# Kernel optimization log

Measured on AMD Instinct MI355X. Metric: run time of the kernel, lower is better.

The kernel has to match this reference:

```python
import math
import jax, jax.numpy as jnp
import numpy as np

N_HEAD = 16
LORA_SCALE = 16.0 / 8.0  # lora_alpha / r


def lora_linear(x, W, b, A, B):
    # y = x @ W^T + b + scale * (x @ A^T) @ B^T
    base = jnp.einsum('btc,oc->bto', x, W) + b
    low = jnp.einsum('btc,rc->btr', x, A)
    return base + LORA_SCALE * jnp.einsum('btr,or->bto', low, B)


def setup_inputs() -> dict:
    key = jax.random.key(0)
    ks = jax.random.split(key, 8)
    B, T, C = 2, 2048, 1024
    r = 8
    s = 0.02
    return {
        'x': jax.random.normal(ks[0], (B, T, C), jnp.float32),
        'W_attn': jax.random.normal(ks[1], (3 * C, C), jnp.float32) * s,
        'b_attn': jnp.zeros((3 * C,), jnp.float32),
        'A_attn': jax.random.normal(ks[2], (r, C), jnp.float32) * s,
        'B_attn': jax.random.normal(ks[3], (3 * C, r), jnp.float32) * s,
        'W_proj': jax.random.normal(ks[4], (C, C), jnp.float32) * s,
        'b_proj': jnp.zeros((C,), jnp.float32),
        'A_proj': jax.random.normal(ks[5], (r, C), jnp.float32) * s,
        'B_proj': jax.random.normal(ks[6], (C, r), jnp.float32) * s,
    }


def reference(x, W_attn, b_attn, A_attn, B_attn, W_proj, b_proj, A_proj, B_proj):
    B, T, C = x.shape
    H = N_HEAD
    hd = C // H
    qkv = lora_linear(x, W_attn, b_attn, A_attn, B_attn)  # [B,T,3C]
    q, k, v = jnp.split(qkv, 3, axis=2)
    # [B,H,T,hd]
    q = q.reshape(B, T, H, hd).transpose(0, 2, 1, 3)
    k = k.reshape(B, T, H, hd).transpose(0, 2, 1, 3)
    v = v.reshape(B, T, H, hd).transpose(0, 2, 1, 3)
    att = jnp.einsum('bhqd,bhkd->bhqk', q, k) * (1.0 / math.sqrt(hd))
    causal = jnp.tril(jnp.ones((T, T), bool))
    att = jnp.where(causal, att, -jnp.inf)
    att = jax.nn.softmax(att, axis=-1)
    out = jnp.einsum('bhqk,bhkd->bhqd', att, v)
    out = out.transpose(0, 2, 1, 3).reshape(B, T, C)
    return lora_linear(out, W_proj, b_proj, A_proj, B_proj)
```

## Files before the change

kernel.cpp:

```cpp
#include <hip/hip_runtime.h>
#include <hip/hip_bf16.h>
#include <stdint.h>

typedef __bf16 bf16_t;
typedef __bf16 bf16x8 __attribute__((ext_vector_type(8)));
typedef __bf16 bf16x4 __attribute__((ext_vector_type(4)));
typedef __bf16 bf16x2 __attribute__((ext_vector_type(2)));
typedef float f32x4 __attribute__((ext_vector_type(4)));
typedef float f32x16 __attribute__((ext_vector_type(16)));
typedef uint32_t u32;
typedef uint32_t u32x4 __attribute__((ext_vector_type(4)));

typedef __attribute__((address_space(1))) void as1void;
typedef __attribute__((address_space(3))) void as3void;

#define QSCALE 0.18033688011112042f

__constant__ unsigned char kOrder[24] = {7, 20, 22, 23, 6, 16, 18, 19, 21,
                                         5, 12, 14, 15, 17, 4, 8, 10, 11, 13,
                                         3, 9, 2, 1, 0};

__device__ __forceinline__ void gll16(const void* g, void* l) {
  __builtin_amdgcn_global_load_lds((as1void*)g, (as3void*)l, 16, 0, 0);
}

__device__ __forceinline__ u32 pack2(float a, float b) {
  bf16x2 t = {(bf16_t)a, (bf16_t)b};
  return __builtin_bit_cast(u32, t);
}

__global__ void prep_all(const float* __restrict__ W_attn, const float* __restrict__ B_attn,
                         const float* __restrict__ A_attn, const float* __restrict__ W_proj,
                         const float* __restrict__ B_proj, const float* __restrict__ A_proj,
                         const float4* __restrict__ x,
                         bf16_t* __restrict__ WaE, bf16_t* __restrict__ WpE,
                         bf16x4* __restrict__ Xb) {
  int bid = blockIdx.x;
  if (bid < 16384) {
    int idx = bid * 256 + threadIdx.x;
    const float *W, *Bm, *Am;
    bf16_t* dst;
    if (idx < 3145728) {
      W = W_attn; Bm = B_attn; Am = A_attn; dst = WaE;
    } else {
      idx -= 3145728;
      W = W_proj; Bm = B_proj; Am = A_proj; dst = WpE;
    }
    int o = idx >> 10, c = idx & 1023;
    float acc = W[idx];
#pragma unroll
    for (int r = 0; r < 8; ++r)
      acc += 2.0f * Bm[o * 8 + r] * Am[r * 1024 + c];
    dst[idx] = (bf16_t)acc;
  } else {
    int i = (bid - 16384) * 256 + threadIdx.x;
    float4 v = x[i];
    bf16x4 o = {(bf16_t)v.x, (bf16_t)v.y, (bf16_t)v.z, (bf16_t)v.w};
    Xb[i] = o;
  }
}

template <bool QKV>
__global__ __launch_bounds__(256, 3) void gemm_bt(
    const bf16_t* __restrict__ A, const bf16_t* __restrict__ Bt,
    const float* __restrict__ bias,
    bf16_t* __restrict__ Qb, bf16_t* __restrict__ Kb, bf16_t* __restrict__ Vb,
    float* __restrict__ Out) {
  __shared__ bf16_t Als[128][64];
  __shared__ bf16_t Bls[128][64];
  const int m0 = blockIdx.x * 128;
  const int n0 = blockIdx.y * 128;
  const int tid = threadIdx.x;
  const int lane = tid & 63;
  const int w = tid >> 6;
  const int wm = w >> 1, wn = w & 1;
  const int lr = lane & 15, g = lane >> 4;
  const int sw = (lane & 7) << 3;
  const int srow = lane >> 3;
  const int soff = ((lane & 7) ^ srow) * 8;

  f32x4 acc[4][4] = {};

  for (int k0 = 0; k0 < 1024; k0 += 64) {
#pragma unroll
    for (int c = 0; c < 4; ++c) {
      int r = w * 32 + c * 8 + srow;
      gll16(A + (size_t)(m0 + r) * 1024 + k0 + soff, &Als[w * 32 + c * 8][0]);
      gll16(Bt + (size_t)(n0 + r) * 1024 + k0 + soff, &Bls[w * 32 + c * 8][0]);
    }
    __syncthreads();
#pragma unroll
    for (int ks = 0; ks < 2; ++ks) {
      bf16x8 af[4], bfv[4];
#pragma unroll
      for (int i = 0; i < 4; ++i)
        af[i] = *(const bf16x8*)&Als[wm * 64 + i * 16 + lr][(ks * 32 + g * 8) ^ sw];
#pragma unroll
      for (int j = 0; j < 4; ++j)
        bfv[j] = *(const bf16x8*)&Bls[wn * 64 + j * 16 + lr][(ks * 32 + g * 8) ^ sw];
#pragma unroll
      for (int i = 0; i < 4; ++i)
#pragma unroll
        for (int j = 0; j < 4; ++j)
          acc[i][j] = __builtin_amdgcn_mfma_f32_16x16x32_bf16(af[i], bfv[j], acc[i][j], 0, 0, 0);
    }
    __syncthreads();
  }

#pragma unroll
  for (int i = 0; i < 4; ++i) {
#pragma unroll
    for (int j = 0; j < 4; ++j) {
#pragma unroll
      for (int e = 0; e < 4; ++e) {
        int m = m0 + wm * 64 + i * 16 + g * 4 + e;
        int n = n0 + wn * 64 + j * 16 + lr;
        float v = acc[i][j][e] + bias[n];
        if (QKV) {
          int b = m >> 11, t = m & 2047;
          int which = n >> 10, hn = n & 1023;
          int h = hn >> 6, d = hn & 63;
          if (which == 0) v *= QSCALE;
          bf16_t* dst = (which == 0) ? Qb : (which == 1) ? Kb : Vb;
          dst[(((size_t)(b * 16 + h)) * 2048 + t) * 64 + d] = (bf16_t)v;
        } else {
          Out[(size_t)m * 1024 + n] = v;
        }
      }
    }
  }
}

__global__ __launch_bounds__(256, 2) void attn_fwd(
    const bf16_t* __restrict__ Qb, const bf16_t* __restrict__ Kb,
    const bf16_t* __restrict__ Vb, bf16_t* __restrict__ Ob,
    bf16_t* __restrict__ Po, float* __restrict__ Pml) {
  __shared__ bf16_t Kls[2][128][64];
  __shared__ bf16_t Vt[2][64][128];

  int id = blockIdx.x;
  int xcd = id & 7, r = id >> 3;
  int bh = xcd * 4 + (r & 3);
  int j = kOrder[r >> 2];
  int qb, kt0, kt1, part;
  if (j < 8) {
    qb = j; kt0 = 0; kt1 = qb + 1; part = -1;
  } else {
    qb = 8 + ((j - 8) >> 1);
    part = (j - 8) & 1;
    int kts = qb + 1, nA = (kts + 1) >> 1;
    kt0 = part ? nA : 0;
    kt1 = part ? kts : nA;
  }
  int b = bh >> 4, h = bh & 15;

  const int tid = threadIdx.x, lane = tid & 63, w = tid >> 6;
  const int q32 = lane & 31;
  const int hi = lane >> 5;
  const int ksw = (q32 & 7) << 3;
  const int vkey = ((q32 & 7) ^ (q32 >> 2)) << 3;
  const bf16_t* Qp = Qb + (size_t)bh * 2048 * 64;
  const bf16_t* Kp = Kb + (size_t)bh * 2048 * 64;
  const bf16_t* Vp = Vb + (size_t)bh * 2048 * 64;

  const int q0 = qb * 128;
  const int qrow = q0 + w * 32 + q32;

  const int kbase = (tid >> 4) * 8;
  const int dbase = (tid & 15) * 4;
  const int ksr = lane >> 3;
  const int kso = ((lane & 7) ^ ksr) * 8;

  bf16x8 qf[4];
#pragma unroll
  for (int ds = 0; ds < 4; ++ds)
    qf[ds] = *(const bf16x8*)(Qp + (size_t)qrow * 64 + ds * 16 + hi * 8);

  float m_run = -3e38f, l_run = 0.f;
  f32x16 o_acc[2] = {};

  {
    const int kp = kt0 * 128;
    uint2 rowv[8];
#pragma unroll
    for (int rr = 0; rr < 8; ++rr)
      rowv[rr] = *(const uint2*)(Vp + (size_t)(kp + kbase + rr) * 64 + dbase);
#pragma unroll
    for (int c = 0; c < 4; ++c) {
      int rb = w * 32 + c * 8;
      gll16(Kp + (size_t)(kp + rb + ksr) * 64 + kso, &Kls[0][rb][0]);
    }
#pragma unroll
    for (int dd = 0; dd < 4; ++dd) {
      u32 sel = (dd & 1) ? 0x07060302u : 0x05040100u;
      u32 a0 = (dd >> 1) ? rowv[0].y : rowv[0].x;
      u32 a1 = (dd >> 1) ? rowv[1].y : rowv[1].x;
      u32 a2 = (dd >> 1) ? rowv[2].y : rowv[2].x;
      u32 a3 = (dd >> 1) ? rowv[3].y : rowv[3].x;
      u32 a4 = (dd >> 1) ? rowv[4].y : rowv[4].x;
      u32 a5 = (dd >> 1) ? rowv[5].y : rowv[5].x;
      u32 a6 = (dd >> 1) ? rowv[6].y : rowv[6].x;
      u32 a7 = (dd >> 1) ? rowv[7].y : rowv[7].x;
      int4 val;
      val.x = __builtin_amdgcn_perm(a1, a0, sel);
      val.y = __builtin_amdgcn_perm(a3, a2, sel);
      val.z = __builtin_amdgcn_perm(a5, a4, sel);
      val.w = __builtin_amdgcn_perm(a7, a6, sel);
      int d = dbase + dd;
      int key = ((d & 7) ^ ((d >> 2) & 7)) << 3;
      *(int4*)&Vt[0][d][kbase ^ key] = val;
    }
    __syncthreads();
  }

  int cb = 0;
  for (int kt = kt0; kt < kt1; ++kt) {
    const bool haveNext = (kt + 1 < kt1);
    const bool maskt = (kt == qb);
    const int nfa = maskt ? (w + 1) : 4;
    const int nb = cb ^ 1;

    uint2 rowv[8];
    if (haveNext) {
      const int kn = (kt + 1) * 128;
#pragma unroll
      for (int rr = 0; rr < 8; ++rr)
        rowv[rr] = *(const uint2*)(Vp + (size_t)(kn + kbase + rr) * 64 + dbase);
#pragma unroll
      for (int c = 0; c < 4; ++c) {
        int rb = w * 32 + c * 8;
        gll16(Kp + (size_t)(kn + rb + ksr) * 64 + kso, &Kls[nb][rb][0]);
      }
    }

    f32x16 s[4] = {};
    __builtin_amdgcn_s_setprio(1);
#pragma unroll
    for (int fa = 0; fa < 4; ++fa) {
      if (fa < nfa) {
#pragma unroll
        for (int ds = 0; ds < 4; ++ds) {
          bf16x8 kf = *(const bf16x8*)&Kls[cb][fa * 32 + q32][(ds * 16 + hi * 8) ^ ksw];
          s[fa] = __builtin_amdgcn_mfma_f32_32x32x16_bf16(kf, qf[ds], s[fa], 0, 0, 0);
        }
      }
    }
    __builtin_amdgcn_s_setprio(0);

    float mloc = -3e38f;
#pragma unroll
    for (int fa = 0; fa < 4; ++fa) {
      if (fa < nfa) {
        if (maskt && fa == w) {
#pragma unroll
          for (int rr = 0; rr < 16; ++rr) {
            int km = (rr & 3) + 8 * (rr >> 2) + 4 * hi;
            if (km > q32) s[fa][rr] = -3e38f;
          }
        }
#pragma unroll
        for (int rr = 0; rr < 16; ++rr) mloc = fmaxf(mloc, s[fa][rr]);
      }
    }
    mloc = fmaxf(mloc, __shfl_xor(mloc, 32, 64));
    if (!__all(mloc <= m_run + 8.0f)) {
      float mnew = fmaxf(m_run, mloc);
      float rs = __builtin_amdgcn_exp2f(m_run - mnew);
      m_run = mnew;
      l_run *= rs;
      o_acc[0] *= rs;
      o_acc[1] *= rs;
    }

    if (haveNext) {
#pragma unroll
      for (int dd = 0; dd < 4; ++dd) {
        u32 sel = (dd & 1) ? 0x07060302u : 0x05040100u;
        u32 a0 = (dd >> 1) ? rowv[0].y : rowv[0].x;
        u32 a1 = (dd >> 1) ? rowv[1].y : rowv[1].x;
        u32 a2 = (dd >> 1) ? rowv[2].y : rowv[2].x;
        u32 a3 = (dd >> 1) ? rowv[3].y : rowv[3].x;
        u32 a4 = (dd >> 1) ? rowv[4].y : rowv[4].x;
        u32 a5 = (dd >> 1) ? rowv[5].y : rowv[5].x;
        u32 a6 = (dd >> 1) ? rowv[6].y : rowv[6].x;
        u32 a7 = (dd >> 1) ? rowv[7].y : rowv[7].x;
        int4 val;
        val.x = __builtin_amdgcn_perm(a1, a0, sel);
        val.y = __builtin_amdgcn_perm(a3, a2, sel);
        val.z = __builtin_amdgcn_perm(a5, a4, sel);
        val.w = __builtin_amdgcn_perm(a7, a6, sel);
        int d = dbase + dd;
        int key = ((d & 7) ^ ((d >> 2) & 7)) << 3;
        *(int4*)&Vt[nb][d][kbase ^ key] = val;
      }
    }

    float lsum = 0.f;
#pragma unroll
    for (int fa = 0; fa < 4; ++fa) {
      if (fa < nfa) {
        float p[16];
#pragma unroll
        for (int rr = 0; rr < 16; ++rr) {
          p[rr] = __builtin_amdgcn_exp2f(s[fa][rr] - m_run);
          lsum += p[rr];
        }
        u32 x0 = pack2(p[0], p[1]),   x1 = pack2(p[2], p[3]);
        u32 x2 = pack2(p[4], p[5]),   x3 = pack2(p[6], p[7]);
        u32 y0 = pack2(p[8], p[9]),   y1 = pack2(p[10], p[11]);
        u32 y2 = pack2(p[12], p[13]), y3 = pack2(p[14], p[15]);
        u32 z0 = hi ? x0 : x2;
        u32 z1 = hi ? x1 : x3;
        u32 z2 = hi ? y0 : y2;
        u32 z3 = hi ? y1 : y3;
        z0 = (u32)__shfl_xor((int)z0, 32, 64);
        z1 = (u32)__shfl_xor((int)z1, 32, 64);
        z2 = (u32)__shfl_xor((int)z2, 32, 64);
        z3 = (u32)__shfl_xor((int)z3, 32, 64);
        u32x4 pw0 = hi ? (u32x4){z0, z1, x2, x3} : (u32x4){x0, x1, z0, z1};
        u32x4 pw1 = hi ? (u32x4){z2, z3, y2, y3} : (u32x4){y0, y1, z2, z3};
        bf16x8 P0 = __builtin_bit_cast(bf16x8, pw0);
        bf16x8 P1 = __builtin_bit_cast(bf16x8, pw1);
        __builtin_amdgcn_s_setprio(1);
#pragma unroll
        for (int db = 0; db < 2; ++db) {
          int d = db * 32 + q32;
          bf16x8 vf0 = *(const bf16x8*)&Vt[cb][d][(fa * 32 + hi * 8) ^ vkey];
          o_acc[db] = __builtin_amdgcn_mfma_f32_32x32x16_bf16(vf0, P0, o_acc[db], 0, 0, 0);
          bf16x8 vf1 = *(const bf16x8*)&Vt[cb][d][(fa * 32 + 16 + hi * 8) ^ vkey];
          o_acc[db] = __builtin_amdgcn_mfma_f32_32x32x16_bf16(vf1, P1, o_acc[db], 0, 0, 0);
        }
        __builtin_amdgcn_s_setprio(0);
      }
    }
    lsum += __shfl_xor(lsum, 32, 64);
    l_run += lsum;

    __syncthreads();
    cb = nb;
  }

  if (part < 0) {
    float inv = 1.0f / l_run;
    bf16_t* obase = Ob + ((size_t)(b * 2048 + qrow)) * 1024 + h * 64;
#pragma unroll
    for (int db = 0; db < 2; ++db) {
#pragma unroll
      for (int rg = 0; rg < 4; ++rg) {
        bf16x4 ov = {(bf16_t)(o_acc[db][rg * 4 + 0] * inv),
                     (bf16_t)(o_acc[db][rg * 4 + 1] * inv),
                     (bf16_t)(o_acc[db][rg * 4 + 2] * inv),
                     (bf16_t)(o_acc[db][rg * 4 + 3] * inv)};
        *(bf16x4*)(obase + db * 32 + rg * 8 + hi * 4) = ov;
      }
    }
  } else {
    int sidx = bh * 16 + (qb - 8) * 2 + part;
    int prow = w * 32 + q32;
    bf16_t* po = Po + (size_t)sidx * 8192 + prow * 64;
#pragma unroll
    for (int db = 0; db < 2; ++db) {
#pragma unroll
      for (int rg = 0; rg < 4; ++rg) {
        bf16x4 ov = {(bf16_t)o_acc[db][rg * 4 + 0], (bf16_t)o_acc[db][rg * 4 + 1],
                     (bf16_t)o_acc[db][rg * 4 + 2], (bf16_t)o_acc[db][rg * 4 + 3]};
        *(bf16x4*)(po + db * 32 + rg * 8 + hi * 4) = ov;
      }
    }
    if (hi == 0) {
      Pml[sidx * 256 + prow * 2] = m_run;
      Pml[sidx * 256 + prow * 2 + 1] = l_run;
    }
  }
}

__global__ __launch_bounds__(256) void attn_merge(
    const bf16_t* __restrict__ Po, const float* __restrict__ Pml,
    bf16_t* __restrict__ Ob) {
  int blk = blockIdx.x;
  int bh = blk >> 3, qb8 = blk & 7;
  int qb = 8 + qb8;
  int b = bh >> 4, h = bh & 15;
  int sA = bh * 16 + qb8 * 2, sB = sA + 1;
  int t = threadIdx.x;
  int row = t >> 1, c0 = (t & 1) * 32;

  float mA = Pml[sA * 256 + row * 2], lA = Pml[sA * 256 + row * 2 + 1];
  float mB = Pml[sB * 256 + row * 2], lB = Pml[sB * 256 + row * 2 + 1];
  float m = fmaxf(mA, mB);
  float wA = __builtin_amdgcn_exp2f(mA - m);
  float wB = __builtin_amdgcn_exp2f(mB - m);
  float inv = 1.0f / (lA * wA + lB * wB);
  wA *= inv;
  wB *= inv;

  const bf16_t* pa = Po + (size_t)sA * 8192 + row * 64 + c0;
  const bf16_t* pb = Po + (size_t)sB * 8192 + row * 64 + c0;
  bf16_t* ob = Ob + ((size_t)(b * 2048 + qb * 128 + row)) * 1024 + h * 64 + c0;
#pragma unroll
  for (int u = 0; u < 4; ++u) {
    bf16x8 a = *(const bf16x8*)(pa + u * 8);
    bf16x8 c = *(const bf16x8*)(pb + u * 8);
    bf16x8 o;
#pragma unroll
    for (int i = 0; i < 8; ++i)
      o[i] = (bf16_t)((float)a[i] * wA + (float)c[i] * wB);
    *(bf16x8*)(ob + u * 8) = o;
  }
}

extern "C" void kernel_launch(void* const* d_in, const int* in_sizes, int n_in,
                              void* d_out, int out_size, void* d_ws, size_t ws_size,
                              hipStream_t stream) {
  const float* x      = (const float*)d_in[0];
  const float* W_attn = (const float*)d_in[1];
  const float* b_attn = (const float*)d_in[2];
  const float* A_attn = (const float*)d_in[3];
  const float* B_attn = (const float*)d_in[4];
  const float* W_proj = (const float*)d_in[5];
  const float* b_proj = (const float*)d_in[6];
  const float* A_proj = (const float*)d_in[7];
  const float* B_proj = (const float*)d_in[8];
  float* out = (float*)d_out;

  char* ws = (char*)d_ws;
  bf16_t* WaE = (bf16_t*)(ws);
  bf16_t* WpE = (bf16_t*)(ws + 6291456);
  bf16_t* Xb  = (bf16_t*)(ws + 8388608);
  bf16_t* Qb  = (bf16_t*)(ws + 16777216);
  bf16_t* Kb  = (bf16_t*)(ws + 25165824);
  bf16_t* Vb  = (bf16_t*)(ws + 33554432);
  bf16_t* Ob  = (bf16_t*)(ws + 41943040);
  float*  Pml = (float*)(ws);
  bf16_t* Po  = (bf16_t*)(ws + 8388608);

  prep_all<<<20480, 256, 0, stream>>>(W_attn, B_attn, A_attn, W_proj, B_proj, A_proj,
                                      (const float4*)x, WaE, WpE, (bf16x4*)Xb);

  gemm_bt<true><<<dim3(32, 24), 256, 0, stream>>>(Xb, WaE, b_attn, Qb, Kb, Vb, nullptr);
  attn_fwd<<<768, 256, 0, stream>>>(Qb, Kb, Vb, Ob, Po, Pml);
  attn_merge<<<256, 256, 0, stream>>>(Po, Pml, Ob);
  gemm_bt<false><<<dim3(32, 8), 256, 0, stream>>>(Ob, WpE, b_proj, nullptr, nullptr, nullptr, out);
}
```

Measured before the change: 113.0 us.

## Enlarge attention query tile to 256 rows with 512-thread blocks

Attention blocks now process 256 query rows using 8 waves instead of 128 rows with 4 waves. Each staged K/V tile is reused by twice as many queries, so global and LDS traffic per query drops. Causal masking, split-KV partitioning, the V transpose layout and the merge kernel are all adapted to the new tile size. The trade-offs are fewer blocks, more work on diagonal tiles where waves sit idle, and higher register and occupancy pressure.

```diff
diff --git a/kernel.cpp b/kernel.cpp
--- a/kernel.cpp
+++ b/kernel.cpp
@@ -16,9 +16,7 @@
 
 #define QSCALE 0.18033688011112042f
 
-__constant__ unsigned char kOrder[24] = {7, 20, 22, 23, 6, 16, 18, 19, 21,
-                                         5, 12, 14, 15, 17, 4, 8, 10, 11, 13,
-                                         3, 9, 2, 1, 0};
+__constant__ unsigned char kOrder12[12] = {3, 10, 11, 8, 9, 2, 6, 7, 4, 5, 1, 0};
 
 __device__ __forceinline__ void gll16(const void* g, void* l) {
   __builtin_amdgcn_global_load_lds((as1void*)g, (as3void*)l, 16, 0, 0);
@@ -131,7 +129,7 @@
   }
 }
 
-__global__ __launch_bounds__(256, 2) void attn_fwd(
+__global__ __launch_bounds__(512, 4) void attn_fwd(
     const bf16_t* __restrict__ Qb, const bf16_t* __restrict__ Kb,
     const bf16_t* __restrict__ Vb, bf16_t* __restrict__ Ob,
     bf16_t* __restrict__ Po, float* __restrict__ Pml) {
@@ -141,16 +139,15 @@
   int id = blockIdx.x;
   int xcd = id & 7, r = id >> 3;
   int bh = xcd * 4 + (r & 3);
-  int j = kOrder[r >> 2];
+  int j = kOrder12[r >> 2];
   int qb, kt0, kt1, part;
-  if (j < 8) {
-    qb = j; kt0 = 0; kt1 = qb + 1; part = -1;
+  if (j < 4) {
+    qb = j; kt0 = 0; kt1 = 2 * qb + 2; part = -1;
   } else {
-    qb = 8 + ((j - 8) >> 1);
-    part = (j - 8) & 1;
-    int kts = qb + 1, nA = (kts + 1) >> 1;
-    kt0 = part ? nA : 0;
-    kt1 = part ? kts : nA;
+    qb = 4 + ((j - 4) >> 1);
+    part = (j - 4) & 1;
+    kt0 = part ? (qb + 1) : 0;
+    kt1 = part ? (2 * qb + 2) : (qb + 1);
   }
   int b = bh >> 4, h = bh & 15;
 
@@ -158,16 +155,16 @@
   const int q32 = lane & 31;
   const int hi = lane >> 5;
   const int ksw = (q32 & 7) << 3;
-  const int vkey = ((q32 & 7) ^ (q32 >> 2)) << 3;
+  const int vkey = ((q32 ^ (q32 >> 1)) & 7) << 3;
   const bf16_t* Qp = Qb + (size_t)bh * 2048 * 64;
   const bf16_t* Kp = Kb + (size_t)bh * 2048 * 64;
   const bf16_t* Vp = Vb + (size_t)bh * 2048 * 64;
 
-  const int q0 = qb * 128;
+  const int q0 = qb * 256;
   const int qrow = q0 + w * 32 + q32;
 
-  const int kbase = (tid >> 4) * 8;
-  const int dbase = (tid & 15) * 4;
+  const int kbase = (tid >> 5) * 8;
+  const int dbase = (tid & 31) * 2;
   const int ksr = lane >> 3;
   const int kso = ((lane & 7) ^ ksr) * 8;
 
@@ -181,33 +178,25 @@
 
   {
     const int kp = kt0 * 128;
-    uint2 rowv[8];
+    u32 rowv[8];
 #pragma unroll
     for (int rr = 0; rr < 8; ++rr)
-      rowv[rr] = *(const uint2*)(Vp + (size_t)(kp + kbase + rr) * 64 + dbase);
-#pragma unroll
-    for (int c = 0; c < 4; ++c) {
-      int rb = w * 32 + c * 8;
+      rowv[rr] = *(const u32*)(Vp + (size_t)(kp + kbase + rr) * 64 + dbase);
+#pragma unroll
+    for (int c = 0; c < 2; ++c) {
+      int rb = w * 16 + c * 8;
       gll16(Kp + (size_t)(kp + rb + ksr) * 64 + kso, &Kls[0][rb][0]);
     }
 #pragma unroll
-    for (int dd = 0; dd < 4; ++dd) {
-      u32 sel = (dd & 1) ? 0x07060302u : 0x05040100u;
-      u32 a0 = (dd >> 1) ? rowv[0].y : rowv[0].x;
-      u32 a1 = (dd >> 1) ? rowv[1].y : rowv[1].x;
-      u32 a2 = (dd >> 1) ? rowv[2].y : rowv[2].x;
-      u32 a3 = (dd >> 1) ? rowv[3].y : rowv[3].x;
-      u32 a4 = (dd >> 1) ? rowv[4].y : rowv[4].x;
-      u32 a5 = (dd >> 1) ? rowv[5].y : rowv[5].x;
-      u32 a6 = (dd >> 1) ? rowv[6].y : rowv[6].x;
-      u32 a7 = (dd >> 1) ? rowv[7].y : rowv[7].x;
+    for (int dd = 0; dd < 2; ++dd) {
+      u32 sel = dd ? 0x07060302u : 0x05040100u;
       int4 val;
-      val.x = __builtin_amdgcn_perm(a1, a0, sel);
-      val.y = __builtin_amdgcn_perm(a3, a2, sel);
-      val.z = __builtin_amdgcn_perm(a5, a4, sel);
-      val.w = __builtin_amdgcn_perm(a7, a6, sel);
+      val.x = __builtin_amdgcn_perm(rowv[1], rowv[0], sel);
+      val.y = __builtin_amdgcn_perm(rowv[3], rowv[2], sel);
+      val.z = __builtin_amdgcn_perm(rowv[5], rowv[4], sel);
+      val.w = __builtin_amdgcn_perm(rowv[7], rowv[6], sel);
       int d = dbase + dd;
-      int key = ((d & 7) ^ ((d >> 2) & 7)) << 3;
+      int key = ((d ^ (d >> 1)) & 7) << 3;
       *(int4*)&Vt[0][d][kbase ^ key] = val;
     }
     __syncthreads();
@@ -216,19 +205,24 @@
   int cb = 0;
   for (int kt = kt0; kt < kt1; ++kt) {
     const bool haveNext = (kt + 1 < kt1);
-    const bool maskt = (kt == qb);
-    const int nfa = maskt ? (w + 1) : 4;
+    const int dtile = kt - 2 * qb;
+    int nfa;
+    if (dtile < 0) nfa = 4;
+    else if (dtile == 0) nfa = (w < 4) ? (w + 1) : 4;
+    else nfa = (w < 4) ? 0 : (w - 3);
+    const int dfa = (dtile == 0) ? ((w < 4) ? w : -1)
+                                 : ((dtile == 1 && w >= 4) ? (w - 4) : -1);
     const int nb = cb ^ 1;
 
-    uint2 rowv[8];
+    u32 rowv[8];
     if (haveNext) {
       const int kn = (kt + 1) * 128;
 #pragma unroll
       for (int rr = 0; rr < 8; ++rr)
-        rowv[rr] = *(const uint2*)(Vp + (size_t)(kn + kbase + rr) * 64 + dbase);
-#pragma unroll
-      for (int c = 0; c < 4; ++c) {
-        int rb = w * 32 + c * 8;
+        rowv[rr] = *(const u32*)(Vp + (size_t)(kn + kbase + rr) * 64 + dbase);
+#pragma unroll
+      for (int c = 0; c < 2; ++c) {
+        int rb = w * 16 + c * 8;
         gll16(Kp + (size_t)(kn + rb + ksr) * 64 + kso, &Kls[nb][rb][0]);
       }
     }
@@ -251,7 +245,7 @@
 #pragma unroll
     for (int fa = 0; fa < 4; ++fa) {
       if (fa < nfa) {
-        if (maskt && fa == w) {
+        if (fa == dfa) {
 #pragma unroll
           for (int rr = 0; rr < 16; ++rr) {
             int km = (rr & 3) + 8 * (rr >> 2) + 4 * hi;
@@ -274,23 +268,15 @@
 
     if (haveNext) {
 #pragma unroll
-      for (int dd = 0; dd < 4; ++dd) {
-        u32 sel = (dd & 1) ? 0x07060302u : 0x05040100u;
-        u32 a0 = (dd >> 1) ? rowv[0].y : rowv[0].x;
-        u32 a1 = (dd >> 1) ? rowv[1].y : rowv[1].x;
-        u32 a2 = (dd >> 1) ? rowv[2].y : rowv[2].x;
-        u32 a3 = (dd >> 1) ? rowv[3].y : rowv[3].x;
-        u32 a4 = (dd >> 1) ? rowv[4].y : rowv[4].x;
-        u32 a5 = (dd >> 1) ? rowv[5].y : rowv[5].x;
-        u32 a6 = (dd >> 1) ? rowv[6].y : rowv[6].x;
-        u32 a7 = (dd >> 1) ? rowv[7].y : rowv[7].x;
+      for (int dd = 0; dd < 2; ++dd) {
+        u32 sel = dd ? 0x07060302u : 0x05040100u;
         int4 val;
-        val.x = __builtin_amdgcn_perm(a1, a0, sel);
-        val.y = __builtin_amdgcn_perm(a3, a2, sel);
-        val.z = __builtin_amdgcn_perm(a5, a4, sel);
-        val.w = __builtin_amdgcn_perm(a7, a6, sel);
+        val.x = __builtin_amdgcn_perm(rowv[1], rowv[0], sel);
+        val.y = __builtin_amdgcn_perm(rowv[3], rowv[2], sel);
+        val.z = __builtin_amdgcn_perm(rowv[5], rowv[4], sel);
+        val.w = __builtin_amdgcn_perm(rowv[7], rowv[6], sel);
         int d = dbase + dd;
-        int key = ((d & 7) ^ ((d >> 2) & 7)) << 3;
+        int key = ((d ^ (d >> 1)) & 7) << 3;
         *(int4*)&Vt[nb][d][kbase ^ key] = val;
       }
     }
@@ -355,9 +341,9 @@
       }
     }
   } else {
-    int sidx = bh * 16 + (qb - 8) * 2 + part;
+    int sidx = bh * 8 + (qb - 4) * 2 + part;
     int prow = w * 32 + q32;
-    bf16_t* po = Po + (size_t)sidx * 8192 + prow * 64;
+    bf16_t* po = Po + (size_t)sidx * 16384 + prow * 64;
 #pragma unroll
     for (int db = 0; db < 2; ++db) {
 #pragma unroll
@@ -368,8 +354,8 @@
       }
     }
     if (hi == 0) {
-      Pml[sidx * 256 + prow * 2] = m_run;
-      Pml[sidx * 256 + prow * 2 + 1] = l_run;
+      Pml[sidx * 512 + prow * 2] = m_run;
+      Pml[sidx * 512 + prow * 2 + 1] = l_run;
     }
   }
 }
@@ -378,15 +364,14 @@
     const bf16_t* __restrict__ Po, const float* __restrict__ Pml,
     bf16_t* __restrict__ Ob) {
   int blk = blockIdx.x;
-  int bh = blk >> 3, qb8 = blk & 7;
-  int qb = 8 + qb8;
+  int bh = blk >> 2, qb4 = blk & 3;
+  int qb = 4 + qb4;
   int b = bh >> 4, h = bh & 15;
-  int sA = bh * 16 + qb8 * 2, sB = sA + 1;
-  int t = threadIdx.x;
-  int row = t >> 1, c0 = (t & 1) * 32;
-
-  float mA = Pml[sA * 256 + row * 2], lA = Pml[sA * 256 + row * 2 + 1];
-  float mB = Pml[sB * 256 + row * 2], lB = Pml[sB * 256 + row * 2 + 1];
+  int sA = bh * 8 + qb4 * 2, sB = sA + 1;
+  int row = threadIdx.x;
+
+  float mA = Pml[sA * 512 + row * 2], lA = Pml[sA * 512 + row * 2 + 1];
+  float mB = Pml[sB * 512 + row * 2], lB = Pml[sB * 512 + row * 2 + 1];
   float m = fmaxf(mA, mB);
   float wA = __builtin_amdgcn_exp2f(mA - m);
   float wB = __builtin_amdgcn_exp2f(mB - m);
@@ -394,11 +379,11 @@
   wA *= inv;
   wB *= inv;
 
-  const bf16_t* pa = Po + (size_t)sA * 8192 + row * 64 + c0;
-  const bf16_t* pb = Po + (size_t)sB * 8192 + row * 64 + c0;
-  bf16_t* ob = Ob + ((size_t)(b * 2048 + qb * 128 + row)) * 1024 + h * 64 + c0;
-#pragma unroll
-  for (int u = 0; u < 4; ++u) {
+  const bf16_t* pa = Po + (size_t)sA * 16384 + row * 64;
+  const bf16_t* pb = Po + (size_t)sB * 16384 + row * 64;
+  bf16_t* ob = Ob + ((size_t)(b * 2048 + qb * 256 + row)) * 1024 + h * 64;
+#pragma unroll
+  for (int u = 0; u < 8; ++u) {
     bf16x8 a = *(const bf16x8*)(pa + u * 8);
     bf16x8 c = *(const bf16x8*)(pb + u * 8);
     bf16x8 o;
@@ -438,7 +423,7 @@
                                       (const float4*)x, WaE, WpE, (bf16x4*)Xb);
 
   gemm_bt<true><<<dim3(32, 24), 256, 0, stream>>>(Xb, WaE, b_attn, Qb, Kb, Vb, nullptr);
-  attn_fwd<<<768, 256, 0, stream>>>(Qb, Kb, Vb, Ob, Po, Pml);
-  attn_merge<<<256, 256, 0, stream>>>(Po, Pml, Ob);
+  attn_fwd<<<384, 512, 0, stream>>>(Qb, Kb, Vb, Ob, Po, Pml);
+  attn_merge<<<128, 256, 0, stream>>>(Po, Pml, Ob);
   gemm_bt<false><<<dim3(32, 8), 256, 0, stream>>>(Ob, WpE, b_proj, nullptr, nullptr, nullptr, out);
 }
```

After: 181.5 us. 60.6% more time.

## Pre-transpose V globally, DMA it into LDS, and XCD-aware GEMM tile mapping

Applied to the files above, without the earlier changes.

Adds a separate kernel that transposes V into a [bh][d][t] layout. The attention kernel can then load V tiles straight into LDS with global_load_lds instead of register loads plus perm shuffles. The GEMM grids become 1D with a block-to-tile mapping that groups tiles per XCD for L2 locality. The first split-attention partial is written directly into Ob, so the merge reads it back from there, which shrinks the Po scratch. The cost is an extra kernel launch and an extra pass over V through global memory.

```diff
diff --git a/kernel.cpp b/kernel.cpp
--- a/kernel.cpp
+++ b/kernel.cpp
@@ -60,6 +60,32 @@
   }
 }
 
+__global__ __launch_bounds__(256) void transpose_v(
+    const bf16_t* __restrict__ Vb, bf16_t* __restrict__ Vtg) {
+  __shared__ bf16_t Lt[128][72];
+  int blk = blockIdx.x;
+  int bh = blk >> 4, tb = blk & 15;
+  int t0 = tb * 128;
+  int tid = threadIdx.x;
+  {
+    int t = tid >> 1, dc = (tid & 1) * 32;
+    const bf16_t* p = Vb + (size_t)bh * 131072 + (size_t)(t0 + t) * 64 + dc;
+#pragma unroll
+    for (int u = 0; u < 4; ++u)
+      *(bf16x8*)&Lt[t][dc + u * 8] = *(const bf16x8*)(p + u * 8);
+  }
+  __syncthreads();
+  int d = tid & 63, tg = tid >> 6;
+  bf16_t* q = Vtg + (size_t)bh * 131072 + (size_t)d * 2048 + t0 + tg * 32;
+#pragma unroll
+  for (int u = 0; u < 4; ++u) {
+    bf16x8 v;
+#pragma unroll
+    for (int e = 0; e < 8; ++e) v[e] = Lt[tg * 32 + u * 8 + e][d];
+    *(bf16x8*)(q + u * 8) = v;
+  }
+}
+
 template <bool QKV>
 __global__ __launch_bounds__(256, 3) void gemm_bt(
     const bf16_t* __restrict__ A, const bf16_t* __restrict__ Bt,
@@ -68,8 +94,24 @@
     float* __restrict__ Out) {
   __shared__ bf16_t Als[128][64];
   __shared__ bf16_t Bls[128][64];
-  const int m0 = blockIdx.x * 128;
-  const int n0 = blockIdx.y * 128;
+  int mb, nb;
+  if (QKV) {
+    int id = blockIdx.x;
+    int xcd = id & 7, s = id >> 3;
+    int half = s >= 48 ? 1 : 0;
+    int within = s - 48 * half;
+    int cm = within & 7, cn = within >> 3;
+    int chunkIdx = half * 8 + xcd;
+    mb = (chunkIdx & 3) * 8 + cm;
+    nb = (chunkIdx >> 2) * 6 + cn;
+  } else {
+    int id = blockIdx.x;
+    int xcd = id & 7, s = id >> 3;
+    mb = (xcd & 3) * 8 + (s & 7);
+    nb = (xcd >> 2) * 4 + (s >> 3);
+  }
+  const int m0 = mb * 128;
+  const int n0 = nb * 128;
   const int tid = threadIdx.x;
   const int lane = tid & 63;
   const int w = tid >> 6;
@@ -133,7 +175,7 @@
 
 __global__ __launch_bounds__(256, 2) void attn_fwd(
     const bf16_t* __restrict__ Qb, const bf16_t* __restrict__ Kb,
-    const bf16_t* __restrict__ Vb, bf16_t* __restrict__ Ob,
+    const bf16_t* __restrict__ Vtg, bf16_t* __restrict__ Ob,
     bf16_t* __restrict__ Po, float* __restrict__ Pml) {
   __shared__ bf16_t Kls[2][128][64];
   __shared__ bf16_t Vt[2][64][128];
@@ -161,15 +203,20 @@
   const int vkey = ((q32 & 7) ^ (q32 >> 2)) << 3;
   const bf16_t* Qp = Qb + (size_t)bh * 2048 * 64;
   const bf16_t* Kp = Kb + (size_t)bh * 2048 * 64;
-  const bf16_t* Vp = Vb + (size_t)bh * 2048 * 64;
+  const bf16_t* Vtp = Vtg + (size_t)bh * 131072;
 
   const int q0 = qb * 128;
   const int qrow = q0 + w * 32 + q32;
 
-  const int kbase = (tid >> 4) * 8;
-  const int dbase = (tid & 15) * 4;
   const int ksr = lane >> 3;
   const int kso = ((lane & 7) ^ ksr) * 8;
+  int vdo[4];
+#pragma unroll
+  for (int cc = 0; cc < 4; ++cc) {
+    int d = 16 * w + 4 * cc + (lane >> 4);
+    int key = (d & 7) ^ ((d >> 2) & 7);
+    vdo[cc] = d * 2048 + (((lane & 15) ^ key) << 3);
+  }
 
   bf16x8 qf[4];
 #pragma unroll
@@ -181,35 +228,14 @@
 
   {
     const int kp = kt0 * 128;
-    uint2 rowv[8];
-#pragma unroll
-    for (int rr = 0; rr < 8; ++rr)
-      rowv[rr] = *(const uint2*)(Vp + (size_t)(kp + kbase + rr) * 64 + dbase);
 #pragma unroll
     for (int c = 0; c < 4; ++c) {
       int rb = w * 32 + c * 8;
       gll16(Kp + (size_t)(kp + rb + ksr) * 64 + kso, &Kls[0][rb][0]);
     }
 #pragma unroll
-    for (int dd = 0; dd < 4; ++dd) {
-      u32 sel = (dd & 1) ? 0x07060302u : 0x05040100u;
-      u32 a0 = (dd >> 1) ? rowv[0].y : rowv[0].x;
-      u32 a1 = (dd >> 1) ? rowv[1].y : rowv[1].x;
-      u32 a2 = (dd >> 1) ? rowv[2].y : rowv[2].x;
-      u32 a3 = (dd >> 1) ? rowv[3].y : rowv[3].x;
-      u32 a4 = (dd >> 1) ? rowv[4].y : rowv[4].x;
-      u32 a5 = (dd >> 1) ? rowv[5].y : rowv[5].x;
-      u32 a6 = (dd >> 1) ? rowv[6].y : rowv[6].x;
-      u32 a7 = (dd >> 1) ? rowv[7].y : rowv[7].x;
-      int4 val;
-      val.x = __builtin_amdgcn_perm(a1, a0, sel);
-      val.y = __builtin_amdgcn_perm(a3, a2, sel);
-      val.z = __builtin_amdgcn_perm(a5, a4, sel);
-      val.w = __builtin_amdgcn_perm(a7, a6, sel);
-      int d = dbase + dd;
-      int key = ((d & 7) ^ ((d >> 2) & 7)) << 3;
-      *(int4*)&Vt[0][d][kbase ^ key] = val;
-    }
+    for (int cc = 0; cc < 4; ++cc)
+      gll16(Vtp + vdo[cc] + kp, &Vt[0][16 * w + 4 * cc][0]);
     __syncthreads();
   }
 
@@ -220,17 +246,16 @@
     const int nfa = maskt ? (w + 1) : 4;
     const int nb = cb ^ 1;
 
-    uint2 rowv[8];
     if (haveNext) {
       const int kn = (kt + 1) * 128;
-#pragma unroll
-      for (int rr = 0; rr < 8; ++rr)
-        rowv[rr] = *(const uint2*)(Vp + (size_t)(kn + kbase + rr) * 64 + dbase);
 #pragma unroll
       for (int c = 0; c < 4; ++c) {
         int rb = w * 32 + c * 8;
         gll16(Kp + (size_t)(kn + rb + ksr) * 64 + kso, &Kls[nb][rb][0]);
       }
+#pragma unroll
+      for (int cc = 0; cc < 4; ++cc)
+        gll16(Vtp + vdo[cc] + kn, &Vt[nb][16 * w + 4 * cc][0]);
     }
 
     f32x16 s[4] = {};
@@ -270,29 +295,6 @@
       l_run *= rs;
       o_acc[0] *= rs;
       o_acc[1] *= rs;
-    }
-
-    if (haveNext) {
-#pragma unroll
-      for (int dd = 0; dd < 4; ++dd) {
-        u32 sel = (dd & 1) ? 0x07060302u : 0x05040100u;
-        u32 a0 = (dd >> 1) ? rowv[0].y : rowv[0].x;
-        u32 a1 = (dd >> 1) ? rowv[1].y : rowv[1].x;
-        u32 a2 = (dd >> 1) ? rowv[2].y : rowv[2].x;
-        u32 a3 = (dd >> 1) ? rowv[3].y : rowv[3].x;
-        u32 a4 = (dd >> 1) ? rowv[4].y : rowv[4].x;
-        u32 a5 = (dd >> 1) ? rowv[5].y : rowv[5].x;
-        u32 a6 = (dd >> 1) ? rowv[6].y : rowv[6].x;
-        u32 a7 = (dd >> 1) ? rowv[7].y : rowv[7].x;
-        int4 val;
-        val.x = __builtin_amdgcn_perm(a1, a0, sel);
-        val.y = __builtin_amdgcn_perm(a3, a2, sel);
-        val.z = __builtin_amdgcn_perm(a5, a4, sel);
-        val.w = __builtin_amdgcn_perm(a7, a6, sel);
-        int d = dbase + dd;
-        int key = ((d & 7) ^ ((d >> 2) & 7)) << 3;
-        *(int4*)&Vt[nb][d][kbase ^ key] = val;
-      }
     }
 
     float lsum = 0.f;
@@ -340,6 +342,7 @@
     cb = nb;
   }
 
+  const int prow = w * 32 + q32;
   if (part < 0) {
     float inv = 1.0f / l_run;
     bf16_t* obase = Ob + ((size_t)(b * 2048 + qrow)) * 1024 + h * 64;
@@ -356,8 +359,11 @@
     }
   } else {
     int sidx = bh * 16 + (qb - 8) * 2 + part;
-    int prow = w * 32 + q32;
-    bf16_t* po = Po + (size_t)sidx * 8192 + prow * 64;
+    bf16_t* po = (part == 0)
+        ? Ob + ((size_t)(b * 2048 + qrow)) * 1024 + h * 64
+        : Po + (size_t)(bh * 8 + (qb - 8)) * 8192 + prow * 64;
+    int stride = (part == 0) ? 1 : 1;
+    (void)stride;
 #pragma unroll
     for (int db = 0; db < 2; ++db) {
 #pragma unroll
@@ -394,12 +400,11 @@
   wA *= inv;
   wB *= inv;
 
-  const bf16_t* pa = Po + (size_t)sA * 8192 + row * 64 + c0;
-  const bf16_t* pb = Po + (size_t)sB * 8192 + row * 64 + c0;
   bf16_t* ob = Ob + ((size_t)(b * 2048 + qb * 128 + row)) * 1024 + h * 64 + c0;
+  const bf16_t* pb = Po + (size_t)(bh * 8 + qb8) * 8192 + row * 64 + c0;
 #pragma unroll
   for (int u = 0; u < 4; ++u) {
-    bf16x8 a = *(const bf16x8*)(pa + u * 8);
+    bf16x8 a = *(const bf16x8*)(ob + u * 8);
     bf16x8 c = *(const bf16x8*)(pb + u * 8);
     bf16x8 o;
 #pragma unroll
@@ -431,14 +436,16 @@
   bf16_t* Kb  = (bf16_t*)(ws + 25165824);
   bf16_t* Vb  = (bf16_t*)(ws + 33554432);
   bf16_t* Ob  = (bf16_t*)(ws + 41943040);
-  float*  Pml = (float*)(ws);
-  bf16_t* Po  = (bf16_t*)(ws + 8388608);
+  bf16_t* Vtg = (bf16_t*)(ws + 8388608);
+  bf16_t* Po  = (bf16_t*)(ws);
+  float*  Pml = (float*)(ws + 4194304);
 
   prep_all<<<20480, 256, 0, stream>>>(W_attn, B_attn, A_attn, W_proj, B_proj, A_proj,
                                       (const float4*)x, WaE, WpE, (bf16x4*)Xb);
 
-  gemm_bt<true><<<dim3(32, 24), 256, 0, stream>>>(Xb, WaE, b_attn, Qb, Kb, Vb, nullptr);
-  attn_fwd<<<768, 256, 0, stream>>>(Qb, Kb, Vb, Ob, Po, Pml);
+  gemm_bt<true><<<768, 256, 0, stream>>>(Xb, WaE, b_attn, Qb, Kb, Vb, nullptr);
+  transpose_v<<<512, 256, 0, stream>>>(Vb, Vtg);
+  attn_fwd<<<768, 256, 0, stream>>>(Qb, Kb, Vtg, Ob, Po, Pml);
   attn_merge<<<256, 256, 0, stream>>>(Po, Pml, Ob);
-  gemm_bt<false><<<dim3(32, 8), 256, 0, stream>>>(Ob, WpE, b_proj, nullptr, nullptr, nullptr, out);
-}
+  gemm_bt<false><<<256, 256, 0, stream>>>(Ob, WpE, b_proj, nullptr, nullptr, nullptr, out);
+}
```

After: 119.5 us. +5.7%, slower.
